# Kernel tuning notes

Measured on AMD Instinct MI355X. Metric: run time of the kernel, lower is better.

Reference implementation:

```python
import jax, jax.numpy as jnp
import numpy as np

B, C, H, W = 16, 256, 64, 64
N = 8                      # num_heads
D = C // N                 # key_dim = head_dim = 32
INIT_VAL, HEADS_RANGE = 1.0, 3.0
SCALING = D ** (-0.5)
EPS = 1e-6


def _rel_pos(h, w):
    # RetNetRelPos2d, chunkwise_recurrent=True branch
    ang = 1.0 / 10000 ** jnp.linspace(0.0, 1.0, D // 2)
    ang = jnp.repeat(ang, 2)                                   # [D]
    idx = jnp.arange(h * w, dtype=jnp.float32)
    sin = jnp.sin(idx[:, None] * ang[None, :]).reshape(h, w, D)
    cos = jnp.cos(idx[:, None] * ang[None, :]).reshape(h, w, D)
    decay = jnp.log(1.0 - 2.0 ** (-INIT_VAL - HEADS_RANGE * jnp.arange(N, dtype=jnp.float32) / N))
    def d1(l):
        i = jnp.arange(l, dtype=jnp.float32)
        return jnp.abs(i[:, None] - i[None, :]) * decay[:, None, None]   # [N,l,l]
    return sin, cos, d1(h), d1(w)


def _rotate_every_two(x):
    x1 = x[..., ::2]
    x2 = x[..., 1::2]
    return jnp.stack([-x2, x1], axis=-1).reshape(x.shape)


def _theta_shift(x, sin, cos):
    return x * cos + _rotate_every_two(x) * sin


def _layernorm(x, g, b):
    m = jnp.mean(x, axis=-1, keepdims=True)
    v = jnp.mean((x - m) ** 2, axis=-1, keepdims=True)
    return g * (x - m) * jax.lax.rsqrt(v + EPS) + b


def setup_inputs() -> dict:
    key = jax.random.key(0)
    ks = jax.random.split(key, 8)
    s = 0.02
    def w(k, shape):
        return (jax.random.normal(k, shape, jnp.float32) * s)
    return {
        "x": jax.random.normal(ks[0], (B, C, H, W), jnp.float32),
        "Wq": w(ks[1], (C, C)), "bq": jnp.zeros((C,), jnp.float32),
        "Wk": w(ks[2], (C, C)), "bk": jnp.zeros((C,), jnp.float32),
        "Wv": w(ks[3], (C, C)), "bv": jnp.zeros((C,), jnp.float32),
        "lepe_w": w(ks[4], (5, 5, 1, C)), "lepe_b": jnp.zeros((C,), jnp.float32),
        "Wo": w(ks[5], (C, C)), "bo": jnp.zeros((C,), jnp.float32),
        "Wfc": w(ks[6], (C, C)), "bfc": jnp.zeros((C,), jnp.float32),
        "g1": jnp.ones((C,), jnp.float32), "b1": jnp.zeros((C,), jnp.float32),
        "g2": jnp.ones((C,), jnp.float32), "b2": jnp.zeros((C,), jnp.float32),
    }


def _vrc(x, sin, cos, mask_h, mask_w, Wq, bq, Wk, bk, Wv, bv, lepe_w, lepe_b, Wo, bo):
    # x: [B,H,W,C]
    b, h, w, _ = x.shape
    q = x @ Wq + bq
    k = (x @ Wk + bk) * SCALING
    v = x @ Wv + bv
    # lepe: depthwise 5x5 conv on v (NHWC)
    lepe = jax.lax.conv_general_dilated(
        v, lepe_w, window_strides=(1, 1), padding=((2, 2), (2, 2)),
        dimension_numbers=("NHWC", "HWIO", "NHWC"), feature_group_count=C) + lepe_b
    # [B,N,H,W,D]
    q = q.reshape(b, h, w, N, D).transpose(0, 3, 1, 2, 4)
    k = k.reshape(b, h, w, N, D).transpose(0, 3, 1, 2, 4)
    qr = _theta_shift(q, sin, cos)
    kr = _theta_shift(k, sin, cos)
    # ---- W-axis attention: [B,H,N,W,W] ----
    qr_w = qr.transpose(0, 2, 1, 3, 4)           # [B,H,N,W,D]
    kr_w = kr.transpose(0, 2, 1, 3, 4)
    v5 = v.reshape(b, h, w, N, D).transpose(0, 1, 3, 2, 4)   # [B,H,N,W,D]
    qk_w = jnp.einsum("bhnqd,bhnkd->bhnqk", qr_w, kr_w) + mask_w
    v5 = jnp.einsum("bhnqk,bhnkd->bhnqd", jax.nn.softmax(qk_w, axis=-1), v5)
    # ---- H-axis attention: [B,W,N,H,H] ----
    qr_h = qr.transpose(0, 3, 1, 2, 4)           # [B,W,N,H,D]
    kr_h = kr.transpose(0, 3, 1, 2, 4)
    v6 = v5.transpose(0, 3, 2, 1, 4)             # [B,W,N,H,D]
    qk_h = jnp.einsum("bwnqd,bwnkd->bwnqk", qr_h, kr_h) + mask_h
    out = jnp.einsum("bwnqk,bwnkd->bwnqd", jax.nn.softmax(qk_h, axis=-1), v6)
    out = out.transpose(0, 3, 1, 2, 4).reshape(b, h, w, C)   # [B,H,W,C]
    return (out + lepe) @ Wo + bo


def reference(x, Wq, bq, Wk, bk, Wv, bv, lepe_w, lepe_b, Wo, bo, Wfc, bfc, g1, b1, g2, b2):
    xt = x.transpose(0, 2, 3, 1)                 # [B,H,W,C]
    sin, cos, mask_h, mask_w = _rel_pos(H, W)
    y = _vrc(xt, sin, cos, mask_h, mask_w, Wq, bq, Wk, bk, Wv, bv, lepe_w, lepe_b, Wo, bo)
    xt = _layernorm(xt + y, g1, b1)
    xt = _layernorm(xt + (xt @ Wfc + bfc), g2, b2)
    return xt.transpose(0, 3, 1, 2)              # [B,C,H,W]
```

## Files before the change

kernel.cpp:

```cpp
#include <hip/hip_runtime.h>
#include <math.h>

#define B_ 16
#define C_ 256
#define N_ 8
#define D_ 32
#define M_ (B_*64*64)
#define SCALING 0.17677669529663687f

typedef short  bf16x8 __attribute__((ext_vector_type(8)));
typedef float  f32x4  __attribute__((ext_vector_type(4)));
typedef unsigned short u16x8 __attribute__((ext_vector_type(8)));

__device__ __forceinline__ unsigned short f2bf(float f) {
    unsigned u = __float_as_uint(f);
    u += 0x7fffu + ((u >> 16) & 1u);
    return (unsigned short)(u >> 16);
}
__device__ __forceinline__ float bf2f(unsigned short h) {
    return __uint_as_float(((unsigned)h) << 16);
}
__device__ __forceinline__ void gld16(const void* g, void* l) {
    __builtin_amdgcn_global_load_lds(
        (const __attribute__((address_space(1))) unsigned*)g,
        (__attribute__((address_space(3))) unsigned*)l, 16, 0, 0);
}

__global__ __launch_bounds__(256) void k_tables(float* __restrict__ sint_t,
                                                float* __restrict__ cost_t)
{
    int t = blockIdx.x * 256 + threadIdx.x;
    int d = t >> 12, p = t & 4095;
    int j = d >> 1;
    float ang = (float)pow(10000.0, -(double)j / 15.0);
    float arg = (float)p * ang;
    sint_t[t] = sinf(arg);
    cost_t[t] = cosf(arg);
}

__global__ __launch_bounds__(256) void k_wcvt(
    const float* __restrict__ Wq, const float* __restrict__ Wk,
    const float* __restrict__ Wv, const float* __restrict__ Wo,
    const float* __restrict__ Wfc,
    unsigned short* __restrict__ Wqt, unsigned short* __restrict__ Wkt,
    unsigned short* __restrict__ Wvt, unsigned short* __restrict__ Wot,
    unsigned short* __restrict__ Wfct)
{
    __shared__ float t[32][33];
    int z = blockIdx.z;
    const float* W = z==0?Wq : z==1?Wk : z==2?Wv : z==3?Wo : Wfc;
    unsigned short* Wt = z==0?Wqt : z==1?Wkt : z==2?Wvt : z==3?Wot : Wfct;
    float sc = (z==1) ? SCALING : 1.0f;
    int tx = threadIdx.x & 31, ty = threadIdx.x >> 5;
    int bx = blockIdx.x * 32;
    int by = blockIdx.y * 32;
    #pragma unroll
    for (int j = 0; j < 4; ++j)
        t[ty + j*8][tx] = W[(by + ty + j*8) * 256 + bx + tx];
    __syncthreads();
    #pragma unroll
    for (int j = 0; j < 4; ++j)
        Wt[(bx + ty + j*8) * 256 + by + tx] = f2bf(t[tx][ty + j*8] * sc);
}

__global__ __launch_bounds__(256) void k_prep(const float* __restrict__ x,
                                              float* __restrict__ xt,
                                              unsigned short* __restrict__ xbf)
{
    __shared__ float t[32][33];
    int tx = threadIdx.x & 31, ty = threadIdx.x >> 5;
    int bx = blockIdx.x * 32;
    int by = blockIdx.y * 32;
    size_t bo = (size_t)blockIdx.z * (256*4096);
    #pragma unroll
    for (int j = 0; j < 4; ++j)
        t[ty + j*8][tx] = x[bo + (size_t)(by + ty + j*8) * 4096 + bx + tx];
    __syncthreads();
    #pragma unroll
    for (int j = 0; j < 4; ++j) {
        float v = t[tx][ty + j*8];
        size_t o = bo + (size_t)(bx + ty + j*8) * 256 + by + tx;
        xt[o] = v;
        xbf[o] = f2bf(v);
    }
}

__device__ __forceinline__ void mfma128(
    const unsigned short* A, const unsigned short* Bt, int r0, int c0,
    unsigned short* As, unsigned short* Bs, f32x4 acc[4][4])
{
    const int tid = threadIdx.x;
    const int w = tid >> 6, l = tid & 63;
    const int wr = w >> 1, wc = w & 1;
    const int fr = l & 15, fq = l >> 4;
    const int srow = 32*w + (l >> 2);
    const int skel = (l & 3) * 8;
    for (int kt = 0; kt < 256; kt += 32) {
        __syncthreads();
        gld16(A  + (size_t)(r0 + srow)      * 256 + kt + skel, As + (32*w)    * 32);
        gld16(A  + (size_t)(r0 + srow + 16) * 256 + kt + skel, As + (32*w+16) * 32);
        gld16(Bt + (size_t)(c0 + srow)      * 256 + kt + skel, Bs + (32*w)    * 32);
        gld16(Bt + (size_t)(c0 + srow + 16) * 256 + kt + skel, Bs + (32*w+16) * 32);
        __syncthreads();
        bf16x8 af[4], bfr[4];
        #pragma unroll
        for (int i = 0; i < 4; ++i)
            af[i] = *(const bf16x8*)(As + (wr*64 + i*16 + fr)*32 + fq*8);
        #pragma unroll
        for (int j = 0; j < 4; ++j)
            bfr[j] = *(const bf16x8*)(Bs + (wc*64 + j*16 + fr)*32 + fq*8);
        #pragma unroll
        for (int i = 0; i < 4; ++i)
            #pragma unroll
            for (int j = 0; j < 4; ++j)
                acc[i][j] = __builtin_amdgcn_mfma_f32_16x16x32_bf16(
                    af[i], bfr[j], acc[i][j], 0, 0, 0);
    }
}

__global__ __launch_bounds__(256) void k_qkv(
    const unsigned short* __restrict__ xbf,
    const unsigned short* __restrict__ Wqt, const unsigned short* __restrict__ Wkt,
    const unsigned short* __restrict__ Wvt,
    const float* __restrict__ bq, const float* __restrict__ bk,
    const float* __restrict__ bv,
    unsigned short* __restrict__ qb, unsigned short* __restrict__ kb,
    unsigned short* __restrict__ vb,
    const float* __restrict__ sint_t, const float* __restrict__ cost_t)
{
    __shared__ __align__(16) unsigned short As[4096], Bs[4096];
    int z = blockIdx.z;
    const unsigned short* Bt = z==0?Wqt : z==1?Wkt : Wvt;
    const float* bias = z==0?bq : z==1?bk : bv;
    unsigned short* dst = z==0?qb : z==1?kb : vb;
    int r0 = blockIdx.x * 128, c0 = blockIdx.y * 128;

    f32x4 acc[4][4];
    #pragma unroll
    for (int i = 0; i < 4; ++i)
        #pragma unroll
        for (int j = 0; j < 4; ++j) { f32x4 zr = {0.f,0.f,0.f,0.f}; acc[i][j] = zr; }
    mfma128(xbf, Bt, r0, c0, As, Bs, acc);

    int l = threadIdx.x & 63, w = threadIdx.x >> 6;
    int wr = w>>1, wc = w&1, fr = l&15, fq = l>>4;
    #pragma unroll
    for (int j = 0; j < 4; ++j) {
        int c = c0 + wc*64 + j*16 + fr;
        float bval = bias[c] * (z==1 ? SCALING : 1.0f);
        int n = c >> 5, dl = c & 31;
        #pragma unroll
        for (int i = 0; i < 4; ++i) {
            int rbase = r0 + wr*64 + i*16 + fq*4;
            int b = rbase >> 12;
            int pos0 = rbase & 4095;
            f32x4 v = acc[i][j];
            v[0] += bval; v[1] += bval; v[2] += bval; v[3] += bval;
            if (z < 2) {
                float4 s4 = *(const float4*)(sint_t + dl*4096 + pos0);
                float4 c4 = *(const float4*)(cost_t + dl*4096 + pos0);
                float p0 = __shfl_xor(v[0], 1);
                float p1 = __shfl_xor(v[1], 1);
                float p2 = __shfl_xor(v[2], 1);
                float p3 = __shfl_xor(v[3], 1);
                if (fr & 1) {
                    v[0] = v[0]*c4.x + p0*s4.x;  v[1] = v[1]*c4.y + p1*s4.y;
                    v[2] = v[2]*c4.z + p2*s4.z;  v[3] = v[3]*c4.w + p3*s4.w;
                } else {
                    v[0] = v[0]*c4.x - p0*s4.x;  v[1] = v[1]*c4.y - p1*s4.y;
                    v[2] = v[2]*c4.z - p2*s4.z;  v[3] = v[3]*c4.w - p3*s4.w;
                }
            }
            size_t obase = (size_t)(b*8 + n) * 131072;
            #pragma unroll
            for (int rg = 0; rg < 4; ++rg)
                dst[obase + (size_t)(pos0 + rg)*32 + dl] = f2bf(v[rg]);
        }
    }
}

__global__ __launch_bounds__(256) void k_gemm_bf(
    const unsigned short* __restrict__ A, const unsigned short* __restrict__ Bt,
    const float* __restrict__ bias, float* __restrict__ out)
{
    __shared__ __align__(16) unsigned short As[4096], Bs[4096];
    int r0 = blockIdx.x * 128, c0 = blockIdx.y * 128;
    f32x4 acc[4][4];
    #pragma unroll
    for (int i = 0; i < 4; ++i)
        #pragma unroll
        for (int j = 0; j < 4; ++j) { f32x4 zr = {0.f,0.f,0.f,0.f}; acc[i][j] = zr; }
    mfma128(A, Bt, r0, c0, As, Bs, acc);
    int l = threadIdx.x & 63, w = threadIdx.x >> 6;
    int wr = w>>1, wc = w&1, fr = l&15, fq = l>>4;
    #pragma unroll
    for (int j = 0; j < 4; ++j) {
        int c = c0 + wc*64 + j*16 + fr;
        float bval = bias[c];
        #pragma unroll
        for (int i = 0; i < 4; ++i) {
            int rbase = r0 + wr*64 + i*16 + fq*4;
            #pragma unroll
            for (int rg = 0; rg < 4; ++rg)
                out[(size_t)(rbase + rg)*256 + c] = acc[i][j][rg] + bval;
        }
    }
}

__global__ __launch_bounds__(256) void k_conv(
    const unsigned short* __restrict__ v, const float* __restrict__ cw,
    const float* __restrict__ cb, float* __restrict__ out)
{
    __shared__ float vs[5*68*36];
    __shared__ float wts[25*32];
    int h = blockIdx.x, n = blockIdx.y, b = blockIdx.z;
    int tid = threadIdx.x;
    for (int i = tid; i < 5*68*36; i += 256) vs[i] = 0.f;
    for (int i = tid; i < 800; i += 256) {
        int tap = i >> 5, d = i & 31;
        wts[i] = cw[tap*256 + n*32 + d];
    }
    __syncthreads();
    const unsigned short* vb_ = v + (size_t)((b*8 + n)*64) * 2048;
    #pragma unroll
    for (int it = 0; it < 5; ++it) {
        int f  = tid + it*256;
        int rr = f >> 8;
        int f2 = f & 255;
        int w  = f2 >> 2, d8 = (f2 & 3) * 8;
        int hh = h + rr - 2;
        if (hh >= 0 && hh < 64) {
            u16x8 vv = *(const u16x8*)(vb_ + hh*2048 + w*32 + d8);
            float* dp = vs + (rr*68 + w + 2)*36 + d8;
            #pragma unroll
            for (int e = 0; e < 8; ++e) dp[e] = bf2f(vv[e]);
        }
    }
    __syncthreads();
    int d = tid & 31, wq = tid >> 5;
    float wreg[25];
    #pragma unroll
    for (int t5 = 0; t5 < 25; ++t5) wreg[t5] = wts[t5*32 + d];
    float bias = cb[n*32 + d];
    for (int w = wq; w < 64; w += 8) {
        float acc = bias;
        #pragma unroll
        for (int dy = 0; dy < 5; ++dy)
            #pragma unroll
            for (int dx = 0; dx < 5; ++dx)
                acc = fmaf(vs[(dy*68 + w + dx)*36 + d], wreg[dy*5+dx], acc);
        out[(size_t)((b*64 + h)*64 + w)*256 + n*32 + d] = acc;
    }
}

__global__ __launch_bounds__(256, 3) void k_attn_mfma(
    const unsigned short* __restrict__ Qb, const unsigned short* __restrict__ Kb,
    const unsigned short* Vb, const float* __restrict__ lepe,
    unsigned short* Ob, int dir)
{
    __shared__ unsigned short S[4 * 4864];
    int tid = threadIdx.x;
    int wv = tid >> 6, l = tid & 63;
    int gid = blockIdx.x * 4 + wv;
    int n = (gid >> 6) & 7;
    int c = l & 15, g = l >> 4;
    size_t base; int sstr;
    if (dir == 0) { base = (size_t)gid * 2048;                               sstr = 32;   }
    else          { base = (size_t)(gid >> 6) * 131072 + (size_t)(gid & 63) * 32; sstr = 2048; }

    unsigned short* Vt = S + wv * 4864;
    unsigned short* Ps = Vt + 2304;

    float decayf = (float)log(1.0 - exp2(-1.0 - 3.0 * (double)n / 8.0));

    #pragma unroll
    for (int it = 0; it < 4; ++it) {
        u16x8 vv = *(const u16x8*)(Vb + base + (size_t)l * sstr + it*8);
        #pragma unroll
        for (int e = 0; e < 8; ++e)
            Vt[(it*8 + e)*72 + l] = vv[e];
    }

    bf16x8 qf[4], kf[4];
    #pragma unroll
    for (int i = 0; i < 4; ++i) {
        qf[i] = *(const bf16x8*)(Qb + base + (size_t)(i*16 + c) * sstr + g*8);
        kf[i] = *(const bf16x8*)(Kb + base + (size_t)(i*16 + c) * sstr + g*8);
    }

    f32x4 acc[4][4];
    #pragma unroll
    for (int i = 0; i < 4; ++i)
        #pragma unroll
        for (int j = 0; j < 4; ++j) { f32x4 zr = {0.f,0.f,0.f,0.f}; acc[i][j] = zr; }
    #pragma unroll
    for (int i = 0; i < 4; ++i)
        #pragma unroll
        for (int j = 0; j < 4; ++j)
            acc[i][j] = __builtin_amdgcn_mfma_f32_16x16x32_bf16(
                qf[i], kf[j], acc[i][j], 0, 0, 0);

    float rinv[4][4];
    #pragma unroll
    for (int i = 0; i < 4; ++i) {
        #pragma unroll
        for (int r = 0; r < 4; ++r) {
            float qi = (float)(i*16 + g*4 + r);
            float m = -1e30f;
            #pragma unroll
            for (int j = 0; j < 4; ++j) {
                float ki = (float)(j*16 + c);
                acc[i][j][r] += fabsf(qi - ki) * decayf;
                m = fmaxf(m, acc[i][j][r]);
            }
            m = fmaxf(m, __shfl_xor(m, 1, 16));
            m = fmaxf(m, __shfl_xor(m, 2, 16));
            m = fmaxf(m, __shfl_xor(m, 4, 16));
            m = fmaxf(m, __shfl_xor(m, 8, 16));
            float s = 0.f;
            #pragma unroll
            for (int j = 0; j < 4; ++j) {
                float e = __expf(acc[i][j][r] - m);
                acc[i][j][r] = e;
                s += e;
            }
            s += __shfl_xor(s, 1, 16);
            s += __shfl_xor(s, 2, 16);
            s += __shfl_xor(s, 4, 16);
            s += __shfl_xor(s, 8, 16);
            rinv[i][r] = 1.f / s;
        }
    }

    f32x4 o[4][2];
    #pragma unroll
    for (int i = 0; i < 4; ++i) { f32x4 zr = {0.f,0.f,0.f,0.f}; o[i][0] = zr; o[i][1] = zr; }
    #pragma unroll
    for (int s = 0; s < 2; ++s) {
        #pragma unroll
        for (int i = 0; i < 4; ++i)
            #pragma unroll
            for (int r = 0; r < 4; ++r)
                #pragma unroll
                for (int jj = 0; jj < 2; ++jj)
                    Ps[(i*16 + g*4 + r)*40 + jj*16 + c] = f2bf(acc[i][2*s + jj][r]);
        bf16x8 vf0 = *(const bf16x8*)(Vt + (     c)*72 + s*32 + g*8);
        bf16x8 vf1 = *(const bf16x8*)(Vt + (16 + c)*72 + s*32 + g*8);
        #pragma unroll
        for (int i = 0; i < 4; ++i) {
            bf16x8 pa = *(const bf16x8*)(Ps + (i*16 + c)*40 + g*8);
            o[i][0] = __builtin_amdgcn_mfma_f32_16x16x32_bf16(pa, vf0, o[i][0], 0, 0, 0);
            o[i][1] = __builtin_amdgcn_mfma_f32_16x16x32_bf16(pa, vf1, o[i][1], 0, 0, 0);
        }
    }

    #pragma unroll
    for (int i = 0; i < 4; ++i) {
        #pragma unroll
        for (int r = 0; r < 4; ++r) {
            int q = i*16 + g*4 + r;
            float ri = rinv[i][r];
            if (dir == 0) {
                Ob[base + (size_t)q*32 + c]      = f2bf(o[i][0][r] * ri);
                Ob[base + (size_t)q*32 + 16 + c] = f2bf(o[i][1][r] * ri);
            } else {
                int b = gid >> 9, w2 = gid & 63;
                size_t idx = ((size_t)((b*64 + q)*64 + w2))*256 + n*32 + c;
                Ob[idx]      = f2bf(o[i][0][r] * ri + lepe[idx]);
                Ob[idx + 16] = f2bf(o[i][1][r] * ri + lepe[idx + 16]);
            }
        }
    }
}

template<bool BFOUT>
__global__ __launch_bounds__(256) void k_ln(
    const float* A, const float* __restrict__ Bv,
    const float* __restrict__ g, const float* __restrict__ bb,
    float* out, unsigned short* __restrict__ outbf)
{
    int row  = blockIdx.x * 4 + (threadIdx.x >> 6);
    int lane = threadIdx.x & 63;
    size_t off = (size_t)row * 256 + lane*4;
    float4 a4 = *(const float4*)(A + off);
    float4 b4 = *(const float4*)(Bv + off);
    float v0=a4.x+b4.x, v1=a4.y+b4.y, v2=a4.z+b4.z, v3=a4.w+b4.w;
    float s = v0+v1+v2+v3;
    #pragma unroll
    for (int mm = 1; mm < 64; mm <<= 1) s += __shfl_xor(s, mm, 64);
    float mean = s * (1.0f/256.0f);
    float d0=v0-mean, d1=v1-mean, d2=v2-mean, d3=v3-mean;
    float qq = d0*d0 + d1*d1 + d2*d2 + d3*d3;
    #pragma unroll
    for (int mm = 1; mm < 64; mm <<= 1) qq += __shfl_xor(qq, mm, 64);
    float rstd = rsqrtf(qq * (1.0f/256.0f) + 1e-6f);
    float4 g4  = *(const float4*)(g + lane*4);
    float4 be4 = *(const float4*)(bb + lane*4);
    float o0 = g4.x*d0*rstd + be4.x, o1 = g4.y*d1*rstd + be4.y;
    float o2 = g4.z*d2*rstd + be4.z, o3 = g4.w*d3*rstd + be4.w;
    *(float4*)(out + off) = make_float4(o0, o1, o2, o3);
    if (BFOUT) {
        ushort4 ov = make_ushort4(f2bf(o0), f2bf(o1), f2bf(o2), f2bf(o3));
        *(ushort4*)(outbf + off) = ov;
    }
}

__global__ __launch_bounds__(256) void k_transpose(const float* __restrict__ src,
                                                   float* __restrict__ dst,
                                                   int rows, int cols)
{
    __shared__ float t[32][33];
    int tx = threadIdx.x & 31, ty = threadIdx.x >> 5;
    int bx = blockIdx.x * 32, by = blockIdx.y * 32;
    size_t bo = (size_t)blockIdx.z * rows * cols;
    #pragma unroll
    for (int j = 0; j < 4; ++j)
        t[ty + j*8][tx] = src[bo + (size_t)(by + ty + j*8) * cols + bx + tx];
    __syncthreads();
    #pragma unroll
    for (int j = 0; j < 4; ++j)
        dst[bo + (size_t)(bx + ty + j*8) * rows + by + tx] = t[tx][ty + j*8];
}

extern "C" void kernel_launch(void* const* d_in, const int* in_sizes, int n_in,
                              void* d_out, int out_size, void* d_ws, size_t ws_size,
                              hipStream_t stream)
{
    (void)in_sizes; (void)n_in; (void)out_size;
    const float* x   = (const float*)d_in[0];
    const float* Wq  = (const float*)d_in[1];
    const float* bq  = (const float*)d_in[2];
    const float* Wk  = (const float*)d_in[3];
    const float* bk  = (const float*)d_in[4];
    const float* Wv  = (const float*)d_in[5];
    const float* bv  = (const float*)d_in[6];
    const float* lw  = (const float*)d_in[7];
    const float* lb  = (const float*)d_in[8];
    const float* Wo  = (const float*)d_in[9];
    const float* bo  = (const float*)d_in[10];
    const float* Wfc = (const float*)d_in[11];
    const float* bfc = (const float*)d_in[12];
    const float* g1  = (const float*)d_in[13];
    const float* b1  = (const float*)d_in[14];
    const float* g2  = (const float*)d_in[15];
    const float* b2  = (const float*)d_in[16];
    float* out = (float*)d_out;

    const size_t NBB = 67108864;
    const size_t NEED = 3*NBB + 2*524288 + 5*131072;
    if (ws_size < NEED) return;

    char* wsb = (char*)d_ws;
    float*          xt   = (float*)wsb;
    unsigned short* xbf  = (unsigned short*)(wsb + NBB);
    unsigned short* qb   = (unsigned short*)(wsb + NBB + NBB/2);
    unsigned short* kb   = (unsigned short*)(wsb + 2*NBB);
    unsigned short* vb   = (unsigned short*)(wsb + 2*NBB + NBB/2);
    float*          yb   = (float*)(wsb + NBB + NBB/2);
    float* sint_t = (float*)(wsb + 3*NBB);
    float* cost_t = sint_t + 131072;
    unsigned short* Wqt  = (unsigned short*)(cost_t + 131072);
    unsigned short* Wkt  = Wqt + 65536;
    unsigned short* Wvt  = Wkt + 65536;
    unsigned short* Wot  = Wvt + 65536;
    unsigned short* Wfct = Wot + 65536;

    k_tables<<<512, 256, 0, stream>>>(sint_t, cost_t);
    k_wcvt<<<dim3(8,8,5), 256, 0, stream>>>(Wq,Wk,Wv,Wo,Wfc,
                                            Wqt,Wkt,Wvt,Wot,Wfct);
    k_prep<<<dim3(128,8,16), 256, 0, stream>>>(x, xt, xbf);
    k_qkv<<<dim3(512,2,3), 256, 0, stream>>>(xbf, Wqt,Wkt,Wvt, bq,bk,bv,
                                             qb,kb,vb, sint_t,cost_t);
    k_conv<<<dim3(64,8,16), 256, 0, stream>>>(vb, lw, lb, out);
    k_attn_mfma<<<2048, 256, 0, stream>>>(qb, kb, vb, nullptr, vb, 0);
    k_attn_mfma<<<2048, 256, 0, stream>>>(qb, kb, vb, out, xbf, 1);
    k_gemm_bf<<<dim3(512,2), 256, 0, stream>>>(xbf, Wot, bo, yb);
    k_ln<true><<<16384, 256, 0, stream>>>(xt, yb, g1, b1, xt, xbf);
    k_gemm_bf<<<dim3(512,2), 256, 0, stream>>>(xbf, Wfct, bfc, out);
    k_ln<false><<<16384, 256, 0, stream>>>(xt, out, g2, b2, yb, nullptr);
    k_transpose<<<dim3(8,128,16), 256, 0, stream>>>(yb, out, 4096, 256);
}
```

Measured before the change: 514.7 us.

## Swizzle LDS GEMM tiles, widen K step, and vectorize transposed epilogue stores

The shared MFMA GEMM helper now stages 64-wide K slices with an XOR-swizzled LDS layout, which halves the number of barriers and is meant to avoid bank conflicts. The MFMA operands are swapped so each lane holds four consecutive output columns. This lets the QKV and output GEMM epilogues use float4 bias loads, vector stores, and rotary pairs computed within the lane instead of through shuffles. The sin/cos tables are re-laid out position-major to match, and LDS per block doubles, which may reduce occupancy.

Result: no change. 519.8 us (+1.0%).

```diff
diff --git a/kernel.cpp b/kernel.cpp
--- a/kernel.cpp
+++ b/kernel.cpp
@@ -26,16 +26,16 @@
         (__attribute__((address_space(3))) unsigned*)l, 16, 0, 0);
 }
 
-__global__ __launch_bounds__(256) void k_tables(float* __restrict__ sint_t,
-                                                float* __restrict__ cost_t)
+__global__ __launch_bounds__(256) void k_tables(float* __restrict__ sint,
+                                                float* __restrict__ cost)
 {
     int t = blockIdx.x * 256 + threadIdx.x;
-    int d = t >> 12, p = t & 4095;
+    int p = t >> 5, d = t & 31;
     int j = d >> 1;
     float ang = (float)pow(10000.0, -(double)j / 15.0);
     float arg = (float)p * ang;
-    sint_t[t] = sinf(arg);
-    cost_t[t] = cosf(arg);
+    sint[t] = sinf(arg);
+    cost[t] = cosf(arg);
 }
 
 __global__ __launch_bounds__(256) void k_wcvt(
@@ -93,28 +93,36 @@
     const int w = tid >> 6, l = tid & 63;
     const int wr = w >> 1, wc = w & 1;
     const int fr = l & 15, fq = l >> 4;
-    const int srow = 32*w + (l >> 2);
-    const int skel = (l & 3) * 8;
-    for (int kt = 0; kt < 256; kt += 32) {
+    const int lrow  = l >> 3;
+    const int lunit = (l & 7) ^ lrow;
+    const int sw = fr & 7;
+    #pragma unroll
+    for (int kt = 0; kt < 256; kt += 64) {
         __syncthreads();
-        gld16(A  + (size_t)(r0 + srow)      * 256 + kt + skel, As + (32*w)    * 32);
-        gld16(A  + (size_t)(r0 + srow + 16) * 256 + kt + skel, As + (32*w+16) * 32);
-        gld16(Bt + (size_t)(c0 + srow)      * 256 + kt + skel, Bs + (32*w)    * 32);
-        gld16(Bt + (size_t)(c0 + srow + 16) * 256 + kt + skel, Bs + (32*w+16) * 32);
+        #pragma unroll
+        for (int it = 0; it < 4; ++it) {
+            int R0 = 32*w + it*8;
+            gld16(A  + (size_t)(r0 + R0 + lrow) * 256 + kt + lunit*8, As + R0*64);
+            gld16(Bt + (size_t)(c0 + R0 + lrow) * 256 + kt + lunit*8, Bs + R0*64);
+        }
         __syncthreads();
-        bf16x8 af[4], bfr[4];
-        #pragma unroll
-        for (int i = 0; i < 4; ++i)
-            af[i] = *(const bf16x8*)(As + (wr*64 + i*16 + fr)*32 + fq*8);
-        #pragma unroll
-        for (int j = 0; j < 4; ++j)
-            bfr[j] = *(const bf16x8*)(Bs + (wc*64 + j*16 + fr)*32 + fq*8);
-        #pragma unroll
-        for (int i = 0; i < 4; ++i)
+        #pragma unroll
+        for (int kk = 0; kk < 2; ++kk) {
+            const int u = (kk*4 + fq) ^ sw;
+            bf16x8 af[4], bfr[4];
+            #pragma unroll
+            for (int i = 0; i < 4; ++i)
+                af[i] = *(const bf16x8*)(As + (wr*64 + i*16 + fr)*64 + u*8);
             #pragma unroll
             for (int j = 0; j < 4; ++j)
-                acc[i][j] = __builtin_amdgcn_mfma_f32_16x16x32_bf16(
-                    af[i], bfr[j], acc[i][j], 0, 0, 0);
+                bfr[j] = *(const bf16x8*)(Bs + (wc*64 + j*16 + fr)*64 + u*8);
+            #pragma unroll
+            for (int i = 0; i < 4; ++i)
+                #pragma unroll
+                for (int j = 0; j < 4; ++j)
+                    acc[i][j] = __builtin_amdgcn_mfma_f32_16x16x32_bf16(
+                        bfr[j], af[i], acc[i][j], 0, 0, 0);
+        }
     }
 }
 
@@ -126,9 +134,9 @@
     const float* __restrict__ bv,
     unsigned short* __restrict__ qb, unsigned short* __restrict__ kb,
     unsigned short* __restrict__ vb,
-    const float* __restrict__ sint_t, const float* __restrict__ cost_t)
-{
-    __shared__ __align__(16) unsigned short As[4096], Bs[4096];
+    const float* __restrict__ sint, const float* __restrict__ cost)
+{
+    __shared__ __align__(16) unsigned short As[8192], Bs[8192];
     int z = blockIdx.z;
     const unsigned short* Bt = z==0?Wqt : z==1?Wkt : Wvt;
     const float* bias = z==0?bq : z==1?bk : bv;
@@ -143,38 +151,30 @@
     mfma128(xbf, Bt, r0, c0, As, Bs, acc);
 
     int l = threadIdx.x & 63, w = threadIdx.x >> 6;
-    int wr = w>>1, wc = w&1, fr = l&15, fq = l>>4;
-    #pragma unroll
-    for (int j = 0; j < 4; ++j) {
-        int c = c0 + wc*64 + j*16 + fr;
-        float bval = bias[c] * (z==1 ? SCALING : 1.0f);
-        int n = c >> 5, dl = c & 31;
-        #pragma unroll
-        for (int i = 0; i < 4; ++i) {
-            int rbase = r0 + wr*64 + i*16 + fq*4;
-            int b = rbase >> 12;
-            int pos0 = rbase & 4095;
+    int wr = w>>1, wc = w&1, c = l&15, g = l>>4;
+    float sc = (z==1) ? SCALING : 1.0f;
+    #pragma unroll
+    for (int i = 0; i < 4; ++i) {
+        int rbase = r0 + wr*64 + i*16 + c;
+        int b = rbase >> 12, pos = rbase & 4095;
+        #pragma unroll
+        for (int j = 0; j < 4; ++j) {
+            int nb = c0 + wc*64 + j*16 + g*4;
+            int nh = nb >> 5, dl = nb & 31;
+            float4 b4 = *(const float4*)(bias + nb);
             f32x4 v = acc[i][j];
-            v[0] += bval; v[1] += bval; v[2] += bval; v[3] += bval;
+            v[0] += b4.x*sc; v[1] += b4.y*sc; v[2] += b4.z*sc; v[3] += b4.w*sc;
             if (z < 2) {
-                float4 s4 = *(const float4*)(sint_t + dl*4096 + pos0);
-                float4 c4 = *(const float4*)(cost_t + dl*4096 + pos0);
-                float p0 = __shfl_xor(v[0], 1);
-                float p1 = __shfl_xor(v[1], 1);
-                float p2 = __shfl_xor(v[2], 1);
-                float p3 = __shfl_xor(v[3], 1);
-                if (fr & 1) {
-                    v[0] = v[0]*c4.x + p0*s4.x;  v[1] = v[1]*c4.y + p1*s4.y;
-                    v[2] = v[2]*c4.z + p2*s4.z;  v[3] = v[3]*c4.w + p3*s4.w;
-                } else {
-                    v[0] = v[0]*c4.x - p0*s4.x;  v[1] = v[1]*c4.y - p1*s4.y;
-                    v[2] = v[2]*c4.z - p2*s4.z;  v[3] = v[3]*c4.w - p3*s4.w;
-                }
+                float4 s4 = *(const float4*)(sint + (size_t)pos*32 + dl);
+                float4 c4 = *(const float4*)(cost + (size_t)pos*32 + dl);
+                float e0 = v[0]*c4.x - v[1]*s4.x;
+                float o0 = v[1]*c4.y + v[0]*s4.y;
+                float e1 = v[2]*c4.z - v[3]*s4.z;
+                float o1 = v[3]*c4.w + v[2]*s4.w;
+                v[0]=e0; v[1]=o0; v[2]=e1; v[3]=o1;
             }
-            size_t obase = (size_t)(b*8 + n) * 131072;
-            #pragma unroll
-            for (int rg = 0; rg < 4; ++rg)
-                dst[obase + (size_t)(pos0 + rg)*32 + dl] = f2bf(v[rg]);
+            ushort4 ov = make_ushort4(f2bf(v[0]), f2bf(v[1]), f2bf(v[2]), f2bf(v[3]));
+            *(ushort4*)(dst + (size_t)(b*8 + nh)*131072 + (size_t)pos*32 + dl) = ov;
         }
     }
 }
@@ -183,7 +183,7 @@
     const unsigned short* __restrict__ A, const unsigned short* __restrict__ Bt,
     const float* __restrict__ bias, float* __restrict__ out)
 {
-    __shared__ __align__(16) unsigned short As[4096], Bs[4096];
+    __shared__ __align__(16) unsigned short As[8192], Bs[8192];
     int r0 = blockIdx.x * 128, c0 = blockIdx.y * 128;
     f32x4 acc[4][4];
     #pragma unroll
@@ -192,17 +192,17 @@
         for (int j = 0; j < 4; ++j) { f32x4 zr = {0.f,0.f,0.f,0.f}; acc[i][j] = zr; }
     mfma128(A, Bt, r0, c0, As, Bs, acc);
     int l = threadIdx.x & 63, w = threadIdx.x >> 6;
-    int wr = w>>1, wc = w&1, fr = l&15, fq = l>>4;
-    #pragma unroll
-    for (int j = 0; j < 4; ++j) {
-        int c = c0 + wc*64 + j*16 + fr;
-        float bval = bias[c];
-        #pragma unroll
-        for (int i = 0; i < 4; ++i) {
-            int rbase = r0 + wr*64 + i*16 + fq*4;
-            #pragma unroll
-            for (int rg = 0; rg < 4; ++rg)
-                out[(size_t)(rbase + rg)*256 + c] = acc[i][j][rg] + bval;
+    int wr = w>>1, wc = w&1, c = l&15, g = l>>4;
+    #pragma unroll
+    for (int i = 0; i < 4; ++i) {
+        int m = r0 + wr*64 + i*16 + c;
+        #pragma unroll
+        for (int j = 0; j < 4; ++j) {
+            int nb = c0 + wc*64 + j*16 + g*4;
+            float4 b4 = *(const float4*)(bias + nb);
+            f32x4 v = acc[i][j];
+            float4 o4 = make_float4(v[0]+b4.x, v[1]+b4.y, v[2]+b4.z, v[3]+b4.w);
+            *(float4*)(out + (size_t)m*256 + nb) = o4;
         }
     }
 }
@@ -457,20 +457,20 @@
     unsigned short* kb   = (unsigned short*)(wsb + 2*NBB);
     unsigned short* vb   = (unsigned short*)(wsb + 2*NBB + NBB/2);
     float*          yb   = (float*)(wsb + NBB + NBB/2);
-    float* sint_t = (float*)(wsb + 3*NBB);
-    float* cost_t = sint_t + 131072;
-    unsigned short* Wqt  = (unsigned short*)(cost_t + 131072);
+    float* sint = (float*)(wsb + 3*NBB);
+    float* cost = sint + 131072;
+    unsigned short* Wqt  = (unsigned short*)(cost + 131072);
     unsigned short* Wkt  = Wqt + 65536;
     unsigned short* Wvt  = Wkt + 65536;
     unsigned short* Wot  = Wvt + 65536;
     unsigned short* Wfct = Wot + 65536;
 
-    k_tables<<<512, 256, 0, stream>>>(sint_t, cost_t);
+    k_tables<<<512, 256, 0, stream>>>(sint, cost);
     k_wcvt<<<dim3(8,8,5), 256, 0, stream>>>(Wq,Wk,Wv,Wo,Wfc,
                                             Wqt,Wkt,Wvt,Wot,Wfct);
     k_prep<<<dim3(128,8,16), 256, 0, stream>>>(x, xt, xbf);
     k_qkv<<<dim3(512,2,3), 256, 0, stream>>>(xbf, Wqt,Wkt,Wvt, bq,bk,bv,
-                                             qb,kb,vb, sint_t,cost_t);
+                                             qb,kb,vb, sint,cost);
     k_conv<<<dim3(64,8,16), 256, 0, stream>>>(vb, lw, lb, out);
     k_attn_mfma<<<2048, 256, 0, stream>>>(qb, kb, vb, nullptr, vb, 0);
     k_attn_mfma<<<2048, 256, 0, stream>>>(qb, kb, vb, out, xbf, 1);
```
